# Kernel optimization log

Measured on AMD Instinct MI355X. Metric: run time of the kernel, lower is better.

Reference implementation:

```python
import jax, jax.numpy as jnp
import numpy as np
from jax import lax

B, T, C, H, K = 8, 4096, 512, 512, 2


def setup_inputs() -> dict:
    key = jax.random.key(0)
    ks = jax.random.split(key, 4)
    scale = 1.0 / np.sqrt(K * C)
    return {
        "x": jax.random.normal(ks[0], (B, T, C), jnp.float32),
        "z_kernel": jax.random.normal(ks[1], (K, C, H), jnp.float32) * scale,
        "z_bias": jnp.zeros((H,), jnp.float32),
        "f_kernel": jax.random.normal(ks[2], (K, C, H), jnp.float32) * scale,
        "f_bias": jnp.zeros((H,), jnp.float32),
        "o_kernel": jax.random.normal(ks[3], (K, C, H), jnp.float32) * scale,
        "o_bias": jnp.zeros((H,), jnp.float32),
    }


def _conv1d(x, kernel, bias):
    # x: [B, T, C]; kernel: [K, C, H] (WIO); causal-left-padded input, VALID conv
    y = lax.conv_general_dilated(
        x, kernel, window_strides=(1,), padding="VALID",
        dimension_numbers=("NWC", "WIO", "NWC"))
    return y + bias


def reference(x, z_kernel, z_bias, f_kernel, f_bias, o_kernel, o_bias):
    k = z_kernel.shape[0]
    xp = jnp.pad(x, ((0, 0), (k - 1, 0), (0, 0)))  # causal pad on time axis
    z = jnp.tanh(_conv1d(xp, z_kernel, z_bias))            # [B, T, H]
    f = jax.nn.sigmoid(_conv1d(xp, f_kernel, f_bias))      # [B, T, H]
    o = jax.nn.sigmoid(_conv1d(xp, o_kernel, o_bias))      # [B, T, H]
    zin = (1.0 - f) * z  # fo-pooling: input gated by (1 - f)

    def step(h, zf):
        z_t, f_t = zf
        h_next = f_t * h + z_t
        return h_next, h_next

    init = jnp.zeros((x.shape[0], z.shape[-1]), z.dtype)
    _, hs = lax.scan(step, init, (jnp.swapaxes(zin, 0, 1), jnp.swapaxes(f, 0, 1)))
    hs = jnp.swapaxes(hs, 0, 1)  # [B, T, H]
    return hs * o
```

## Files before the change

kernel.cpp:

```cpp
#include <hip/hip_runtime.h>
#include <hip/hip_fp16.h>
#include <stdint.h>

#define Bb 8
#define Tt 4096
#define Cc 512
#define Hh 512
#define Mm (Bb*Tt)
#define Nn (3*Hh)
#define Kk (2*Cc)
#define NC 256
#define LC (Tt/NC)
#define XBS (Tt*Cc + Cc)
#define BK 64

typedef _Float16 half8 __attribute__((ext_vector_type(8)));
typedef _Float16 half4 __attribute__((ext_vector_type(4)));
typedef float  floatx4 __attribute__((ext_vector_type(4)));

typedef const __attribute__((address_space(1))) uint32_t* gptr_t;
typedef __attribute__((address_space(3))) uint32_t* lptr_t;

__device__ __forceinline__ void g2lds16(const void* g, void* l) {
    __builtin_amdgcn_global_load_lds((gptr_t)g, (lptr_t)l, 16, 0, 0);
}

__device__ __forceinline__ float fsigmoid(float x) {
    return 1.0f / (1.0f + __expf(-x));
}
__device__ __forceinline__ float ftanh(float x) {
    return 2.0f / (1.0f + __expf(-2.0f * x)) - 1.0f;
}

__global__ __launch_bounds__(256) void cvt_x(const float* __restrict__ x,
                                             _Float16* __restrict__ xh) {
    long i4 = ((long)blockIdx.x * 256 + threadIdx.x) * 4;
    int b = blockIdx.y;
    if (i4 >= XBS) return;
    half4 v;
    if (i4 >= Cc) {
        floatx4 xx = *(const floatx4*)&x[(long)b * (Tt*Cc) + i4 - Cc];
        v[0] = (_Float16)xx[0]; v[1] = (_Float16)xx[1];
        v[2] = (_Float16)xx[2]; v[3] = (_Float16)xx[3];
    } else {
        v[0] = v[1] = v[2] = v[3] = (_Float16)0.0f;
    }
    *(half4*)&xh[(long)b * XBS + i4] = v;
}

__global__ __launch_bounds__(256) void cvt_w(const float* __restrict__ zk,
                                             const float* __restrict__ fk,
                                             const float* __restrict__ ok,
                                             _Float16* __restrict__ bt) {
    __shared__ float tile[64][65];
    const int c0 = (blockIdx.x & 7) * 64;
    const int h0 = (blockIdx.x >> 3) * 64;
    const int which = blockIdx.y >> 1;
    const int kw    = blockIdx.y & 1;
    const float* src = (which == 0) ? zk : ((which == 1) ? fk : ok);
    src += kw * (Cc * Hh);
    const int tr  = threadIdx.x >> 4;
    const int tc4 = (threadIdx.x & 15) * 4;
#pragma unroll
    for (int i = 0; i < 4; ++i) {
        int c = tr + i * 16;
        floatx4 v = *(const floatx4*)&src[(long)(c0 + c) * Hh + h0 + tc4];
        tile[c][tc4 + 0] = v[0]; tile[c][tc4 + 1] = v[1];
        tile[c][tc4 + 2] = v[2]; tile[c][tc4 + 3] = v[3];
    }
    __syncthreads();
#pragma unroll
    for (int i = 0; i < 4; ++i) {
        int h = tr + i * 16;
        half4 o;
#pragma unroll
        for (int j = 0; j < 4; ++j) o[j] = (_Float16)tile[tc4 + j][h];
        *(half4*)&bt[((long)(which * 512 + h0 + h) << 10) + kw * 512 + c0 + tc4] = o;
    }
}

__global__ __launch_bounds__(256, 3) void gemm_qrnn(const _Float16* __restrict__ xh,
                                                    const _Float16* __restrict__ bt,
                                                    const float* __restrict__ zb,
                                                    const float* __restrict__ fb,
                                                    const float* __restrict__ ob,
                                                    _Float16* __restrict__ yh) {
    __shared__ _Float16 lA[128 * BK];
    __shared__ _Float16 lB[128 * BK];

    const int tid  = threadIdx.x;
    const int lane = tid & 63;
    const int w    = tid >> 6;
    const int m0   = blockIdx.x * 128;
    const int n0   = blockIdx.y * 128;
    const int wm   = (w & 1) * 64;
    const int wn   = (w >> 1) * 64;
    const int q    = lane >> 4;
    const int l15  = lane & 15;

    const int rl = lane >> 3;
    const int j  = lane & 7;
    const int jx = (j ^ rl) * 8;

    const _Float16* asrc[4];
    const _Float16* bsrc[4];
    _Float16* adst[4];
    _Float16* bdst[4];
#pragma unroll
    for (int i = 0; i < 4; ++i) {
        int r0 = w * 32 + i * 8;
        int rgA = m0 + r0 + rl;
        asrc[i] = xh + (((long)(rgA + (rgA >> 12))) << 9) + jx;
        int rgB = n0 + r0 + rl;
        bsrc[i] = bt + (((long)rgB) << 10) + jx;
        adst[i] = &lA[r0 * BK];
        bdst[i] = &lB[r0 * BK];
    }

    int aaddr[4], baddr[4];
    const int psw = (q ^ (l15 & 7)) * 8;
#pragma unroll
    for (int i = 0; i < 4; ++i) {
        aaddr[i] = (wm + i * 16 + l15) * BK + psw;
        baddr[i] = (wn + i * 16 + l15) * BK + psw;
    }

    floatx4 acc[4][4] = {};

    for (int kt = 0; kt < Kk / BK; ++kt) {
        const int kb = kt * BK;
#pragma unroll
        for (int i = 0; i < 4; ++i) g2lds16(asrc[i] + kb, adst[i]);
#pragma unroll
        for (int i = 0; i < 4; ++i) g2lds16(bsrc[i] + kb, bdst[i]);
        __syncthreads();

        half8 a0[4], a1[4], b0[4], b1[4];
#pragma unroll
        for (int i = 0; i < 4; ++i) {
            a0[i] = *(const half8*)&lA[aaddr[i]];
            a1[i] = *(const half8*)&lA[aaddr[i] ^ 32];
            b0[i] = *(const half8*)&lB[baddr[i]];
            b1[i] = *(const half8*)&lB[baddr[i] ^ 32];
        }
#pragma unroll
        for (int mi = 0; mi < 4; ++mi)
#pragma unroll
            for (int ni = 0; ni < 4; ++ni)
                acc[mi][ni] = __builtin_amdgcn_mfma_f32_16x16x32_f16(
                    a0[mi], b0[ni], acc[mi][ni], 0, 0, 0);
#pragma unroll
        for (int mi = 0; mi < 4; ++mi)
#pragma unroll
            for (int ni = 0; ni < 4; ++ni)
                acc[mi][ni] = __builtin_amdgcn_mfma_f32_16x16x32_f16(
                    a1[mi], b1[ni], acc[mi][ni], 0, 0, 0);
        __syncthreads();
    }

    const int gate = n0 >> 9;
    const float* bias = (gate == 0) ? zb : ((gate == 1) ? fb : ob);
    float bv[4];
#pragma unroll
    for (int ni = 0; ni < 4; ++ni)
        bv[ni] = bias[(n0 & 511) + wn + ni * 16 + l15];

#pragma unroll
    for (int mi = 0; mi < 4; ++mi) {
#pragma unroll
        for (int ni = 0; ni < 4; ++ni) {
#pragma unroll
            for (int r = 0; r < 4; ++r) {
                int m = m0 + wm + mi * 16 + q * 4 + r;
                int n = n0 + wn + ni * 16 + l15;
                float v = acc[mi][ni][r] + bv[ni];
                float a = (gate == 0) ? ftanh(v) : fsigmoid(v);
                yh[(long)m * Nn + n] = (_Float16)a;
            }
        }
    }
}

__global__ __launch_bounds__(64) void scan_partial(const _Float16* __restrict__ yh,
                                                   float* __restrict__ pf,
                                                   float* __restrict__ he) {
    int c = blockIdx.x & (NC - 1);
    int b = blockIdx.x >> 8;
    int lane = threadIdx.x;
    long base = ((long)(b * Tt + c * LC)) * Nn + lane * 8;
    float hl[8] = {0,0,0,0,0,0,0,0};
    float p[8]  = {1,1,1,1,1,1,1,1};
#pragma unroll 4
    for (int t = 0; t < LC; ++t) {
        half8 z8 = *(const half8*)&yh[base];
        half8 f8 = *(const half8*)&yh[base + 512];
#pragma unroll
        for (int jj = 0; jj < 8; ++jj) {
            float f = (float)f8[jj];
            hl[jj] = f * hl[jj] + (1.0f - f) * (float)z8[jj];
            p[jj] *= f;
        }
        base += Nn;
    }
    long o = ((long)(b * NC + c)) * Hh + lane * 8;
#pragma unroll
    for (int jj = 0; jj < 8; ++jj) { pf[o + jj] = p[jj]; he[o + jj] = hl[jj]; }
}

__global__ __launch_bounds__(256) void scan_combine(const float* __restrict__ pf,
                                                    const float* __restrict__ he,
                                                    float* __restrict__ hin) {
    int idx = blockIdx.x * 256 + threadIdx.x;
    int b = idx >> 9;
    int h = idx & 511;
    float hcur = 0.0f;
#pragma unroll 8
    for (int c = 0; c < NC; ++c) {
        int o = (b * NC + c) * Hh + h;
        hin[o] = hcur;
        hcur = pf[o] * hcur + he[o];
    }
}

__global__ __launch_bounds__(64) void scan_final(const _Float16* __restrict__ yh,
                                                 const float* __restrict__ hin,
                                                 float* __restrict__ out) {
    int c = blockIdx.x & (NC - 1);
    int b = blockIdx.x >> 8;
    int lane = threadIdx.x;
    long base  = ((long)(b * Tt + c * LC)) * Nn + lane * 8;
    long obase = ((long)(b * Tt + c * LC)) * Hh + lane * 8;
    long hb = ((long)(b * NC + c)) * Hh + lane * 8;
    float h[8];
#pragma unroll
    for (int jj = 0; jj < 8; ++jj) h[jj] = hin[hb + jj];
#pragma unroll 4
    for (int t = 0; t < LC; ++t) {
        half8 z8 = *(const half8*)&yh[base];
        half8 f8 = *(const half8*)&yh[base + 512];
        half8 o8 = *(const half8*)&yh[base + 1024];
#pragma unroll
        for (int jj = 0; jj < 8; ++jj) {
            float f = (float)f8[jj];
            h[jj] = f * h[jj] + (1.0f - f) * (float)z8[jj];
            out[obase + jj] = h[jj] * (float)o8[jj];
        }
        base += Nn;
        obase += Hh;
    }
}

extern "C" void kernel_launch(void* const* d_in, const int* in_sizes, int n_in,
                              void* d_out, int out_size, void* d_ws, size_t ws_size,
                              hipStream_t stream) {
    const float* x  = (const float*)d_in[0];
    const float* zk = (const float*)d_in[1];
    const float* zbias = (const float*)d_in[2];
    const float* fk = (const float*)d_in[3];
    const float* fbias = (const float*)d_in[4];
    const float* ok = (const float*)d_in[5];
    const float* obias = (const float*)d_in[6];
    float* out = (float*)d_out;

    char* ws = (char*)d_ws;
    _Float16* xh = (_Float16*)ws;
    _Float16* bt = (_Float16*)(ws + 33562624);
    _Float16* yh = (_Float16*)(ws + 36708352);
    float*    pf = (float*)(ws);
    float*    he = (float*)(ws + 4194304);
    float*    hin= (float*)(ws + 8388608);

    cvt_x<<<dim3((XBS/4 + 255) / 256, Bb), 256, 0, stream>>>(x, xh);
    cvt_w<<<dim3(64, 6), 256, 0, stream>>>(zk, fk, ok, bt);
    gemm_qrnn<<<dim3(Mm / 128, Nn / 128), 256, 0, stream>>>(xh, bt, zbias, fbias, obias, yh);
    scan_partial<<<dim3(Bb * NC), 64, 0, stream>>>(yh, pf, he);
    scan_combine<<<dim3(16), 256, 0, stream>>>(pf, he, hin);
    scan_final<<<dim3(Bb * NC), 64, 0, stream>>>(yh, hin, out);
}
```

Before: 308.1 us.

## Triple-buffer GEMM LDS with 256x128 tiles, 8 waves, and XCD-aware block swizzle

Reworks the fused conv GEMM to use 256x128 tiles with 512 threads. Global-to-LDS loads go into a three-stage ring buffer held in dynamic shared memory, so the loads for tile t+2 are issued while tile t is being computed. MFMA work is split into two barrier-delimited phases, raised with s_setprio, and controlled with explicit vmcnt waits. Block indices are remapped so that neighbouring tiles land on the same XCD for L2 reuse. The scan_combine launch is also spread over more, smaller blocks; in exchange the kernel uses more LDS, which lowers occupancy, and the hand-written waitcnt synchronisation is fragile.

```diff
diff --git a/kernel.cpp b/kernel.cpp
--- a/kernel.cpp
+++ b/kernel.cpp
@@ -13,6 +13,10 @@
 #define LC (Tt/NC)
 #define XBS (Tt*Cc + Cc)
 #define BK 64
+#define NT (Kk/BK)
+#define ABUF 16384
+#define TBUF 24576
+#define LDS_BYTES (3 * TBUF * 2)
 
 typedef _Float16 half8 __attribute__((ext_vector_type(8)));
 typedef _Float16 half4 __attribute__((ext_vector_type(4)));
@@ -79,42 +83,93 @@
     }
 }
 
-__global__ __launch_bounds__(256, 3) void gemm_qrnn(const _Float16* __restrict__ xh,
+
+#define WGBAR() do { __builtin_amdgcn_sched_barrier(0); \
+                     __builtin_amdgcn_s_barrier(); \
+                     __builtin_amdgcn_sched_barrier(0); } while (0)
+
+#define MFMA16(d, av, bv) d = __builtin_amdgcn_mfma_f32_16x16x32_f16(av, bv, d, 0, 0, 0)
+
+#define STAGE_A(s, boff) { _Pragma("unroll") \
+    for (int i_ = 0; i_ < 4; ++i_) g2lds16(asrc[i_] + (s) * 64, &ls[(boff) + adst[i_]]); }
+#define STAGE_B(s, boff) { _Pragma("unroll") \
+    for (int i_ = 0; i_ < 2; ++i_) g2lds16(bsrc[i_] + (s) * 64, &ls[(boff) + bdst[i_]]); }
+
+#define PHASE_A(CB, DOSTAGE) { \
+    _Pragma("unroll") for (int mi = 0; mi < 4; ++mi) { \
+        a0[mi] = *(const half8*)&ls[(CB) + aaddr[mi]]; \
+        a1[mi] = *(const half8*)&ls[(CB) + (aaddr[mi] ^ 32)]; } \
+    half8 b0[2], b1[2]; \
+    _Pragma("unroll") for (int ni = 0; ni < 2; ++ni) { \
+        b0[ni] = *(const half8*)&ls[(CB) + baddr[ni]]; \
+        b1[ni] = *(const half8*)&ls[(CB) + (baddr[ni] ^ 32)]; } \
+    DOSTAGE; \
+    WGBAR(); \
+    __builtin_amdgcn_s_setprio(1); \
+    _Pragma("unroll") for (int mi = 0; mi < 4; ++mi) { \
+        MFMA16(acc[mi][0], a0[mi], b0[0]); \
+        MFMA16(acc[mi][0], a1[mi], b1[0]); \
+        MFMA16(acc[mi][1], a0[mi], b0[1]); \
+        MFMA16(acc[mi][1], a1[mi], b1[1]); } \
+    __builtin_amdgcn_s_setprio(0); \
+    WGBAR(); }
+
+#define PHASE_B(CB, DOSTAGE, GATE) { \
+    half8 b0[2], b1[2]; \
+    _Pragma("unroll") for (int ni = 0; ni < 2; ++ni) { \
+        b0[ni] = *(const half8*)&ls[(CB) + baddr[2 + ni]]; \
+        b1[ni] = *(const half8*)&ls[(CB) + (baddr[2 + ni] ^ 32)]; } \
+    DOSTAGE; \
+    GATE; \
+    WGBAR(); \
+    __builtin_amdgcn_s_setprio(1); \
+    _Pragma("unroll") for (int mi = 0; mi < 4; ++mi) { \
+        MFMA16(acc[mi][2], a0[mi], b0[0]); \
+        MFMA16(acc[mi][2], a1[mi], b1[0]); \
+        MFMA16(acc[mi][3], a0[mi], b0[1]); \
+        MFMA16(acc[mi][3], a1[mi], b1[1]); } \
+    __builtin_amdgcn_s_setprio(0); \
+    WGBAR(); }
+
+__global__ __launch_bounds__(512, 2) void gemm_qrnn(const _Float16* __restrict__ xh,
                                                     const _Float16* __restrict__ bt,
                                                     const float* __restrict__ zb,
                                                     const float* __restrict__ fb,
                                                     const float* __restrict__ ob,
                                                     _Float16* __restrict__ yh) {
-    __shared__ _Float16 lA[128 * BK];
-    __shared__ _Float16 lB[128 * BK];
+    extern __shared__ _Float16 ls[];
 
     const int tid  = threadIdx.x;
     const int lane = tid & 63;
     const int w    = tid >> 6;
-    const int m0   = blockIdx.x * 128;
-    const int n0   = blockIdx.y * 128;
-    const int wm   = (w & 1) * 64;
-    const int wn   = (w >> 1) * 64;
-    const int q    = lane >> 4;
-    const int l15  = lane & 15;
-
-    const int rl = lane >> 3;
-    const int j  = lane & 7;
-    const int jx = (j ^ rl) * 8;
-
-    const _Float16* asrc[4];
-    const _Float16* bsrc[4];
-    _Float16* adst[4];
-    _Float16* bdst[4];
+
+    const int bid = blockIdx.x;
+    const int wg  = (bid & 7) * 192 + (bid >> 3);
+    const int m0  = (wg / 12) * 256;
+    const int n0  = (wg % 12) * 128;
+
+    const int wm  = (w & 3) * 64;
+    const int wn  = (w >> 2) * 64;
+    const int q   = lane >> 4;
+    const int l15 = lane & 15;
+    const int rl  = lane >> 3;
+    const int j   = lane & 7;
+    const int jx  = (j ^ rl) * 8;
+
+    const _Float16* asrc[4]; int adst[4];
 #pragma unroll
     for (int i = 0; i < 4; ++i) {
-        int r0 = w * 32 + i * 8;
+        int r0  = w * 32 + i * 8;
         int rgA = m0 + r0 + rl;
         asrc[i] = xh + (((long)(rgA + (rgA >> 12))) << 9) + jx;
-        int rgB = n0 + r0 + rl;
-        bsrc[i] = bt + (((long)rgB) << 10) + jx;
-        adst[i] = &lA[r0 * BK];
-        bdst[i] = &lB[r0 * BK];
+        adst[i] = r0 * BK;
+    }
+    const _Float16* bsrc[2]; int bdst[2];
+#pragma unroll
+    for (int i = 0; i < 2; ++i) {
+        int r0 = w * 16 + i * 8;
+        bsrc[i] = bt + (((long)(n0 + r0 + rl)) << 10) + jx;
+        bdst[i] = ABUF + r0 * BK;
     }
 
     int aaddr[4], baddr[4];
@@ -122,41 +177,29 @@
 #pragma unroll
     for (int i = 0; i < 4; ++i) {
         aaddr[i] = (wm + i * 16 + l15) * BK + psw;
-        baddr[i] = (wn + i * 16 + l15) * BK + psw;
+        baddr[i] = ABUF + (wn + i * 16 + l15) * BK + psw;
     }
 
     floatx4 acc[4][4] = {};
-
-    for (int kt = 0; kt < Kk / BK; ++kt) {
-        const int kb = kt * BK;
-#pragma unroll
-        for (int i = 0; i < 4; ++i) g2lds16(asrc[i] + kb, adst[i]);
-#pragma unroll
-        for (int i = 0; i < 4; ++i) g2lds16(bsrc[i] + kb, bdst[i]);
-        __syncthreads();
-
-        half8 a0[4], a1[4], b0[4], b1[4];
-#pragma unroll
-        for (int i = 0; i < 4; ++i) {
-            a0[i] = *(const half8*)&lA[aaddr[i]];
-            a1[i] = *(const half8*)&lA[aaddr[i] ^ 32];
-            b0[i] = *(const half8*)&lB[baddr[i]];
-            b1[i] = *(const half8*)&lB[baddr[i] ^ 32];
-        }
-#pragma unroll
-        for (int mi = 0; mi < 4; ++mi)
-#pragma unroll
-            for (int ni = 0; ni < 4; ++ni)
-                acc[mi][ni] = __builtin_amdgcn_mfma_f32_16x16x32_f16(
-                    a0[mi], b0[ni], acc[mi][ni], 0, 0, 0);
-#pragma unroll
-        for (int mi = 0; mi < 4; ++mi)
-#pragma unroll
-            for (int ni = 0; ni < 4; ++ni)
-                acc[mi][ni] = __builtin_amdgcn_mfma_f32_16x16x32_f16(
-                    a1[mi], b1[ni], acc[mi][ni], 0, 0, 0);
-        __syncthreads();
-    }
+    half8 a0[4], a1[4];
+
+    STAGE_A(0, 0);      STAGE_B(0, 0);
+    STAGE_A(1, TBUF);   STAGE_B(1, TBUF);
+    asm volatile("s_waitcnt vmcnt(6)" ::: "memory");
+    WGBAR();
+
+    int cb = 0, nb = TBUF, sb = 2 * TBUF;
+    for (int t = 0; t < NT - 2; ++t) {
+        PHASE_A(cb, STAGE_A(t + 2, sb));
+        PHASE_B(cb, STAGE_B(t + 2, sb),
+                asm volatile("s_waitcnt vmcnt(6)" ::: "memory"));
+        int tmp = cb; cb = nb; nb = sb; sb = tmp;
+    }
+    PHASE_A(cb, );
+    PHASE_B(cb, , asm volatile("s_waitcnt vmcnt(0)" ::: "memory"));
+    cb = nb;
+    PHASE_A(cb, );
+    PHASE_B(cb, , );
 
     const int gate = n0 >> 9;
     const float* bias = (gate == 0) ? zb : ((gate == 1) ? fb : ob);
@@ -207,10 +250,10 @@
     for (int jj = 0; jj < 8; ++jj) { pf[o + jj] = p[jj]; he[o + jj] = hl[jj]; }
 }
 
-__global__ __launch_bounds__(256) void scan_combine(const float* __restrict__ pf,
-                                                    const float* __restrict__ he,
-                                                    float* __restrict__ hin) {
-    int idx = blockIdx.x * 256 + threadIdx.x;
+__global__ __launch_bounds__(64) void scan_combine(const float* __restrict__ pf,
+                                                   const float* __restrict__ he,
+                                                   float* __restrict__ hin) {
+    int idx = blockIdx.x * 64 + threadIdx.x;
     int b = idx >> 9;
     int h = idx & 511;
     float hcur = 0.0f;
@@ -270,10 +313,16 @@
     float*    he = (float*)(ws + 4194304);
     float*    hin= (float*)(ws + 8388608);
 
+    static int once = [](){
+        hipFuncSetAttribute(reinterpret_cast<const void*>(gemm_qrnn),
+                            hipFuncAttributeMaxDynamicSharedMemorySize, LDS_BYTES);
+        return 0; }();
+    (void)once;
+
     cvt_x<<<dim3((XBS/4 + 255) / 256, Bb), 256, 0, stream>>>(x, xh);
     cvt_w<<<dim3(64, 6), 256, 0, stream>>>(zk, fk, ok, bt);
-    gemm_qrnn<<<dim3(Mm / 128, Nn / 128), 256, 0, stream>>>(xh, bt, zbias, fbias, obias, yh);
+    gemm_qrnn<<<dim3((Mm/256) * (Nn/128)), 512, LDS_BYTES, stream>>>(xh, bt, zbias, fbias, obias, yh);
     scan_partial<<<dim3(Bb * NC), 64, 0, stream>>>(yh, pf, he);
-    scan_combine<<<dim3(16), 256, 0, stream>>>(pf, he, hin);
+    scan_combine<<<dim3(64), 64, 0, stream>>>(pf, he, hin);
     scan_final<<<dim3(Bb * NC), 64, 0, stream>>>(yh, hin, out);
 }
```

New measurement: 326.9 us. 1.06x slower.

## Rewrite QRNN GEMM as 256x256 double-buffered ping-pong pipeline with XCD-aware tile mapping

Applied to the files above, without the earlier changes.

Replaces the 128x128 single-buffered GEMM with a 256x256 tile per 512-thread block. It double-buffers LDS through dynamic shared memory and interleaves global-to-LDS staging of the next K tile with MFMA work in four phases, using explicit barriers, setprio and vmcnt waits. Blocks are remapped across the eight XCDs so neighbouring tiles share cache, and the scan_combine launch is reshaped to 64 blocks of 64 threads to spread work over more CUs. This raises register use (32 accumulators per thread) and LDS use (128KB), which lowers occupancy, and the hand-tuned waitcnt schedule is fragile.

```diff
diff --git a/kernel.cpp b/kernel.cpp
--- a/kernel.cpp
+++ b/kernel.cpp
@@ -13,6 +13,10 @@
 #define LC (Tt/NC)
 #define XBS (Tt*Cc + Cc)
 #define BK 64
+#define NT (Kk/BK)
+#define ABUFE 16384
+#define TBUFE 32768
+#define LDSB  (2*TBUFE*2)
 
 typedef _Float16 half8 __attribute__((ext_vector_type(8)));
 typedef _Float16 half4 __attribute__((ext_vector_type(4)));
@@ -79,84 +83,103 @@
     }
 }
 
-__global__ __launch_bounds__(256, 3) void gemm_qrnn(const _Float16* __restrict__ xh,
+
+#define SBAR __builtin_amdgcn_sched_barrier(0)
+#define BARRIER do { SBAR; __builtin_amdgcn_s_barrier(); SBAR; } while (0)
+#define PRIO1 __builtin_amdgcn_s_setprio(1)
+#define PRIO0 __builtin_amdgcn_s_setprio(0)
+#define VM(n) asm volatile("s_waitcnt vmcnt(" #n ")" ::: "memory")
+
+#define RD_A(CB, h) { _Pragma("unroll") for (int mi = 0; mi < 4; ++mi) { \
+    a[mi][0] = *(const half8*)&ls[(CB) + amB  + ((h)*4 + mi) * 1024]; \
+    a[mi][1] = *(const half8*)&ls[(CB) + amBx + ((h)*4 + mi) * 1024]; } }
+
+#define RD_B(dst, CB, h) { _Pragma("unroll") for (int ni = 0; ni < 2; ++ni) { \
+    dst[ni][0] = *(const half8*)&ls[(CB) + bnB  + ((h)*2 + ni) * 1024]; \
+    dst[ni][1] = *(const half8*)&ls[(CB) + bnBx + ((h)*2 + ni) * 1024]; } }
+
+#define STG_A(h, NB, kb) { _Pragma("unroll") for (int i_ = 0; i_ < 2; ++i_) \
+    g2lds16(aptr + ((h)*64 + i_*8) * 512 + (kb), \
+            &ls[(NB) + adstB + ((h)*64 + i_*8) * 64]); }
+
+#define STG_B(h, NB, kb) { _Pragma("unroll") for (int i_ = 0; i_ < 2; ++i_) \
+    g2lds16(bptr + (((long)((h)*32 + i_*8)) << 10) + (kb), \
+            &ls[(NB) + bdstB + ((h)*32 + i_*8) * 64]); }
+
+#define MMQ(mq, nq, bb) { _Pragma("unroll") for (int mi = 0; mi < 4; ++mi) { \
+    _Pragma("unroll") for (int ni = 0; ni < 2; ++ni) { \
+      acc[(mq)+mi][(nq)+ni] = __builtin_amdgcn_mfma_f32_16x16x32_f16( \
+          a[mi][0], bb[ni][0], acc[(mq)+mi][(nq)+ni], 0, 0, 0); \
+      acc[(mq)+mi][(nq)+ni] = __builtin_amdgcn_mfma_f32_16x16x32_f16( \
+          a[mi][1], bb[ni][1], acc[(mq)+mi][(nq)+ni], 0, 0, 0); } } }
+
+#define TILE(CB, NB, kb, DOSTG, G1, G2, G4) { \
+   \
+  RD_A(CB, 0); RD_B(bA, CB, 0); if (DOSTG) { STG_A(0, NB, kb); } \
+  BARRIER; PRIO1; MMQ(0, 0, bA); PRIO0; G1; BARRIER; \
+   \
+  RD_B(bB, CB, 1); if (DOSTG) { STG_B(0, NB, kb); } \
+  BARRIER; PRIO1; MMQ(0, 2, bB); PRIO0; G2; BARRIER; \
+   \
+  RD_A(CB, 1); if (DOSTG) { STG_B(1, NB, kb); } \
+  BARRIER; PRIO1; MMQ(4, 2, bB); PRIO0; BARRIER; \
+   \
+  RD_B(bA, CB, 0); if (DOSTG) { STG_A(1, NB, kb); } \
+  BARRIER; PRIO1; MMQ(4, 0, bA); PRIO0; G4; BARRIER; }
+
+__global__ __launch_bounds__(512, 2) void gemm_qrnn(const _Float16* __restrict__ xh,
                                                     const _Float16* __restrict__ bt,
                                                     const float* __restrict__ zb,
                                                     const float* __restrict__ fb,
                                                     const float* __restrict__ ob,
                                                     _Float16* __restrict__ yh) {
-    __shared__ _Float16 lA[128 * BK];
-    __shared__ _Float16 lB[128 * BK];
+    extern __shared__ _Float16 ls[];
 
     const int tid  = threadIdx.x;
     const int lane = tid & 63;
     const int w    = tid >> 6;
-    const int m0   = blockIdx.x * 128;
-    const int n0   = blockIdx.y * 128;
-    const int wm   = (w & 1) * 64;
-    const int wn   = (w >> 1) * 64;
-    const int q    = lane >> 4;
-    const int l15  = lane & 15;
-
-    const int rl = lane >> 3;
-    const int j  = lane & 7;
-    const int jx = (j ^ rl) * 8;
-
-    const _Float16* asrc[4];
-    const _Float16* bsrc[4];
-    _Float16* adst[4];
-    _Float16* bdst[4];
-#pragma unroll
-    for (int i = 0; i < 4; ++i) {
-        int r0 = w * 32 + i * 8;
-        int rgA = m0 + r0 + rl;
-        asrc[i] = xh + (((long)(rgA + (rgA >> 12))) << 9) + jx;
-        int rgB = n0 + r0 + rl;
-        bsrc[i] = bt + (((long)rgB) << 10) + jx;
-        adst[i] = &lA[r0 * BK];
-        bdst[i] = &lB[r0 * BK];
-    }
-
-    int aaddr[4], baddr[4];
-    const int psw = (q ^ (l15 & 7)) * 8;
-#pragma unroll
-    for (int i = 0; i < 4; ++i) {
-        aaddr[i] = (wm + i * 16 + l15) * BK + psw;
-        baddr[i] = (wn + i * 16 + l15) * BK + psw;
-    }
-
-    floatx4 acc[4][4] = {};
-
-    for (int kt = 0; kt < Kk / BK; ++kt) {
-        const int kb = kt * BK;
-#pragma unroll
-        for (int i = 0; i < 4; ++i) g2lds16(asrc[i] + kb, adst[i]);
-#pragma unroll
-        for (int i = 0; i < 4; ++i) g2lds16(bsrc[i] + kb, bdst[i]);
-        __syncthreads();
-
-        half8 a0[4], a1[4], b0[4], b1[4];
-#pragma unroll
-        for (int i = 0; i < 4; ++i) {
-            a0[i] = *(const half8*)&lA[aaddr[i]];
-            a1[i] = *(const half8*)&lA[aaddr[i] ^ 32];
-            b0[i] = *(const half8*)&lB[baddr[i]];
-            b1[i] = *(const half8*)&lB[baddr[i] ^ 32];
-        }
-#pragma unroll
-        for (int mi = 0; mi < 4; ++mi)
-#pragma unroll
-            for (int ni = 0; ni < 4; ++ni)
-                acc[mi][ni] = __builtin_amdgcn_mfma_f32_16x16x32_f16(
-                    a0[mi], b0[ni], acc[mi][ni], 0, 0, 0);
-#pragma unroll
-        for (int mi = 0; mi < 4; ++mi)
-#pragma unroll
-            for (int ni = 0; ni < 4; ++ni)
-                acc[mi][ni] = __builtin_amdgcn_mfma_f32_16x16x32_f16(
-                    a1[mi], b1[ni], acc[mi][ni], 0, 0, 0);
-        __syncthreads();
-    }
+
+    const int bid = blockIdx.x;
+    const int wg  = (bid & 7) * 96 + (bid >> 3);
+    const int m0  = (wg / 6) * 256;
+    const int n0  = (wg % 6) * 256;
+
+    const int wm  = (w & 1) * 128;
+    const int wn  = (w >> 1) * 64;
+    const int q   = lane >> 4;
+    const int l15 = lane & 15;
+    const int rl  = lane >> 3;
+    const int j   = lane & 7;
+    const int jx  = (j ^ rl) * 8;
+
+    const int aRowBase = (w & 1) * 128 + (w >> 1) * 16;
+    const long rgA0 = (long)m0 + aRowBase + rl;
+    const _Float16* aptr = xh + ((rgA0 + (m0 >> 12)) << 9) + jx;
+    const int adstB = aRowBase * 64;
+    const int bRowBase = (w >> 1) * 64 + (w & 1) * 16;
+    const _Float16* bptr = bt + (((long)(n0 + bRowBase + rl)) << 10) + jx;
+    const int bdstB = ABUFE + bRowBase * 64;
+
+    const int psw  = (q ^ (l15 & 7)) * 8;
+    const int amB  = (wm + l15) * 64 + psw;
+    const int amBx = amB ^ 32;
+    const int bnB  = ABUFE + (wn + l15) * 64 + psw;
+    const int bnBx = bnB ^ 32;
+
+    floatx4 acc[8][4] = {};
+    half8 a[4][2], bA[2][2], bB[2][2];
+
+    STG_A(0, 0, 0); STG_B(0, 0, 0); STG_B(1, 0, 0); STG_A(1, 0, 0);
+    VM(4);
+    BARRIER;
+
+    for (int tp = 0; tp < 7; ++tp) {
+        const int kb0 = (tp * 2 + 1) * 64;
+        TILE(0,     TBUFE, kb0,      true, VM(4), VM(4), VM(4));
+        TILE(TBUFE, 0,     kb0 + 64, true, VM(4), VM(4), VM(4));
+    }
+    TILE(0,     TBUFE, 15 * 64, true,  VM(4), VM(4), VM(4));
+    TILE(TBUFE, 0,     0,       false, VM(2), VM(0), (void)0);
 
     const int gate = n0 >> 9;
     const float* bias = (gate == 0) ? zb : ((gate == 1) ? fb : ob);
@@ -166,7 +189,7 @@
         bv[ni] = bias[(n0 & 511) + wn + ni * 16 + l15];
 
 #pragma unroll
-    for (int mi = 0; mi < 4; ++mi) {
+    for (int mi = 0; mi < 8; ++mi) {
 #pragma unroll
         for (int ni = 0; ni < 4; ++ni) {
 #pragma unroll
@@ -174,8 +197,8 @@
                 int m = m0 + wm + mi * 16 + q * 4 + r;
                 int n = n0 + wn + ni * 16 + l15;
                 float v = acc[mi][ni][r] + bv[ni];
-                float a = (gate == 0) ? ftanh(v) : fsigmoid(v);
-                yh[(long)m * Nn + n] = (_Float16)a;
+                float av = (gate == 0) ? ftanh(v) : fsigmoid(v);
+                yh[(long)m * Nn + n] = (_Float16)av;
             }
         }
     }
@@ -207,10 +230,10 @@
     for (int jj = 0; jj < 8; ++jj) { pf[o + jj] = p[jj]; he[o + jj] = hl[jj]; }
 }
 
-__global__ __launch_bounds__(256) void scan_combine(const float* __restrict__ pf,
-                                                    const float* __restrict__ he,
-                                                    float* __restrict__ hin) {
-    int idx = blockIdx.x * 256 + threadIdx.x;
+__global__ __launch_bounds__(64) void scan_combine(const float* __restrict__ pf,
+                                                   const float* __restrict__ he,
+                                                   float* __restrict__ hin) {
+    int idx = blockIdx.x * 64 + threadIdx.x;
     int b = idx >> 9;
     int h = idx & 511;
     float hcur = 0.0f;
@@ -270,10 +293,16 @@
     float*    he = (float*)(ws + 4194304);
     float*    hin= (float*)(ws + 8388608);
 
+    static int once = [](){
+        hipFuncSetAttribute(reinterpret_cast<const void*>(gemm_qrnn),
+                            hipFuncAttributeMaxDynamicSharedMemorySize, LDSB);
+        return 0; }();
+    (void)once;
+
     cvt_x<<<dim3((XBS/4 + 255) / 256, Bb), 256, 0, stream>>>(x, xh);
     cvt_w<<<dim3(64, 6), 256, 0, stream>>>(zk, fk, ok, bt);
-    gemm_qrnn<<<dim3(Mm / 128, Nn / 128), 256, 0, stream>>>(xh, bt, zbias, fbias, obias, yh);
+    gemm_qrnn<<<dim3((Mm/256) * (Nn/256)), 512, LDSB, stream>>>(xh, bt, zbias, fbias, obias, yh);
     scan_partial<<<dim3(Bb * NC), 64, 0, stream>>>(yh, pf, he);
-    scan_combine<<<dim3(16), 256, 0, stream>>>(pf, he, hin);
+    scan_combine<<<dim3(64), 64, 0, stream>>>(pf, he, hin);
     scan_final<<<dim3(Bb * NC), 64, 0, stream>>>(yh, hin, out);
 }
```

New measurement: 292.1 us. -5.2%, faster.
